# Performance work log

Measured on AMD Instinct MI355X. Metric: run time of the kernel, lower is better.

Reference implementation:

```python
import jax, jax.numpy as jnp
import numpy as np

INTRINSIC_DIM = 3  # all linear dims, no periodic dims
EPS = 1e-10


def _cdist(a, b):
    # Euclidean distance via the expanded form; clamp for numerical safety.
    sq = (jnp.sum(a * a, axis=1)[:, None]
          + jnp.sum(b * b, axis=1)[None, :]
          - 2.0 * (a @ b.T))
    return jnp.sqrt(jnp.maximum(sq, 0.0))


def _thin_plate_kernel(r, dim):
    r_safe = jnp.maximum(r, EPS)
    if dim == 2:
        k = r_safe ** 2 * jnp.log(r_safe)
    else:
        k = r_safe ** (dim - 2) * jnp.log(r_safe)
    return jnp.where(r < EPS, jnp.zeros_like(k), k)


def setup_inputs() -> dict:
    key = jax.random.key(0)
    k1, k2, k3, k4 = jax.random.split(key, 4)
    batch, n, d, amb = 16384, 4096, INTRINSIC_DIM, 3
    m = 1 + d  # constant + one linear term per (non-periodic) dim
    u = jax.random.uniform(k1, (batch, d), dtype=jnp.float32)
    control_points = jax.random.uniform(k2, (n, d), dtype=jnp.float32)
    rbf_weights = jax.random.normal(k3, (n, amb), dtype=jnp.float32)
    poly_coeffs = jax.random.normal(k4, (m, amb), dtype=jnp.float32)
    return {"u": u, "control_points": control_points,
            "rbf_weights": rbf_weights, "poly_coeffs": poly_coeffs}


def reference(u, control_points, rbf_weights, poly_coeffs):
    # K_query: (batch, n) TPS kernel on pairwise Euclidean distances
    dists = _cdist(u, control_points)
    K_query = _thin_plate_kernel(dists, dim=INTRINSIC_DIM)
    # Polynomial matrix: [1, x] over all linear dims -> (batch, 1 + d)
    P_query = jnp.concatenate([jnp.ones((u.shape[0], 1), dtype=u.dtype), u], axis=1)
    return K_query @ rbf_weights + P_query @ poly_coeffs
```

## Files before the change

### kernel.cpp

```cpp
#include <hip/hip_runtime.h>


#define BLK 256
#define NS 4
#define QPT 2
#define QPB 128
#define JCHUNK 256
#define JW (JCHUNK / NS)

__global__ __launch_bounds__(BLK, 8) void tps_kernel(
    const float* __restrict__ u,
    const float* __restrict__ cp,
    const float* __restrict__ w,
    const float* __restrict__ poly,
    float* __restrict__ out,
    int batch, int n)
{
    __shared__ float4 s_a[JCHUNK];
    __shared__ float4 s_b[JCHUNK];
    __shared__ float  s_red[NS][QPB * 3];

    const float C = 0.34657359027997264f;

    const int tid = threadIdx.x;
    const int j0 = blockIdx.y * JCHUNK;

    {
        const int g = j0 + tid;
        const float cx = cp[g * 3 + 0], cy = cp[g * 3 + 1], cz = cp[g * 3 + 2];
        s_a[tid] = make_float4(-2.f * cx, -2.f * cy, -2.f * cz,
                               fmaf(cx, cx, fmaf(cy, cy, cz * cz)));
        s_b[tid] = make_float4(C * w[g * 3 + 0], C * w[g * 3 + 1],
                               C * w[g * 3 + 2], 0.f);
    }
    __syncthreads();

    const int lane = tid & 63;
    const int wv   = tid >> 6;

    float ux[QPT], uy[QPT], uz[QPT], usq[QPT];
    float ax[QPT], ay[QPT], az[QPT];
#pragma unroll
    for (int k = 0; k < QPT; ++k) {
        const int q = blockIdx.x * QPB + k * 64 + lane;
        ux[k] = u[q * 3 + 0];
        uy[k] = u[q * 3 + 1];
        uz[k] = u[q * 3 + 2];
        usq[k] = fmaf(ux[k], ux[k], fmaf(uy[k], uy[k], uz[k] * uz[k]));
        ax[k] = ay[k] = az[k] = 0.f;
    }

    if (blockIdx.y == 0 && wv == 0) {
#pragma unroll
        for (int k = 0; k < QPT; ++k) {
            ax[k] = poly[0] + ux[k] * poly[3] + uy[k] * poly[6] + uz[k] * poly[9];
            ay[k] = poly[1] + ux[k] * poly[4] + uy[k] * poly[7] + uz[k] * poly[10];
            az[k] = poly[2] + ux[k] * poly[5] + uy[k] * poly[8] + uz[k] * poly[11];
        }
    }

    const int jlo = wv * JW;
#pragma unroll 4
    for (int j = jlo; j < jlo + JW; ++j) {
        const float4 A = s_a[j];
        const float4 B = s_b[j];
#pragma unroll
        for (int k = 0; k < QPT; ++k) {
            float r2 = fmaf(A.x, ux[k],
                       fmaf(A.y, uy[k],
                       fmaf(A.z, uz[k], A.w + usq[k])));
            r2 = fmaxf(r2, 1e-30f);
            const float kk = __builtin_amdgcn_sqrtf(r2) *
                             __builtin_amdgcn_logf(r2);
            ax[k] = fmaf(kk, B.x, ax[k]);
            ay[k] = fmaf(kk, B.y, ay[k]);
            az[k] = fmaf(kk, B.z, az[k]);
        }
    }

#pragma unroll
    for (int k = 0; k < QPT; ++k) {
        const int base = (k * 64 + lane) * 3;
        s_red[wv][base + 0] = ax[k];
        s_red[wv][base + 1] = ay[k];
        s_red[wv][base + 2] = az[k];
    }
    __syncthreads();

    for (int v = tid; v < QPB * 3; v += BLK) {
        float s = s_red[0][v] + s_red[1][v] + s_red[2][v] + s_red[3][v];
        atomicAdd(&out[(size_t)blockIdx.x * (QPB * 3) + v], s);
    }
}

extern "C" void kernel_launch(void* const* d_in, const int* in_sizes, int n_in,
                              void* d_out, int out_size, void* d_ws, size_t ws_size,
                              hipStream_t stream) {
    const float* u    = (const float*)d_in[0];
    const float* cp   = (const float*)d_in[1];
    const float* w    = (const float*)d_in[2];
    const float* poly = (const float*)d_in[3];
    float* out = (float*)d_out;

    const int batch = in_sizes[0] / 3;
    const int n     = in_sizes[1] / 3;

    hipMemsetAsync(d_out, 0, (size_t)out_size * sizeof(float), stream);

    dim3 block(BLK);
    dim3 grid(batch / QPB, n / JCHUNK);
    tps_kernel<<<grid, block, 0, stream>>>(u, cp, w, poly, out, batch, n);
}
```

Measured before the change: 80.32 us.

## Precompute packed control-point table and stream it via scalar loads

Adds a small pre-pass kernel that packs the scaled control-point terms and weights into an 8-float-per-point table in workspace. The main kernel then reads that table through wave-uniform scalar loads (s_load_dwordx16) into SGPRs instead of staging through LDS with a block barrier. This removes the per-block shared-memory fill, the __syncthreads and the LDS reads from the inner loop. In exchange it adds an extra kernel launch, and each 4-point group waits on its scalar loads with s_waitcnt lgkmcnt(0) and no prefetching, which can stall the wave.

Result: slower. 83.35 us (+3.8%).

```diff
diff --git a/kernel.cpp b/kernel.cpp
--- a/kernel.cpp
+++ b/kernel.cpp
@@ -8,35 +8,37 @@
 #define JCHUNK 256
 #define JW (JCHUNK / NS)
 
+typedef __attribute__((ext_vector_type(16))) int v16i;
+
+__global__ void pack_kernel(const float* __restrict__ cp,
+                            const float* __restrict__ w,
+                            float* __restrict__ pack, int n) {
+    const int j = blockIdx.x * blockDim.x + threadIdx.x;
+    if (j >= n) return;
+    const float C = 0.34657359027997264f;
+    const float cx = cp[j * 3 + 0], cy = cp[j * 3 + 1], cz = cp[j * 3 + 2];
+    pack[j * 8 + 0] = -2.f * cx;
+    pack[j * 8 + 1] = -2.f * cy;
+    pack[j * 8 + 2] = -2.f * cz;
+    pack[j * 8 + 3] = fmaf(cx, cx, fmaf(cy, cy, cz * cz));
+    pack[j * 8 + 4] = C * w[j * 3 + 0];
+    pack[j * 8 + 5] = C * w[j * 3 + 1];
+    pack[j * 8 + 6] = C * w[j * 3 + 2];
+    pack[j * 8 + 7] = 0.f;
+}
+
 __global__ __launch_bounds__(BLK, 8) void tps_kernel(
     const float* __restrict__ u,
-    const float* __restrict__ cp,
-    const float* __restrict__ w,
+    const float* __restrict__ pack,
     const float* __restrict__ poly,
     float* __restrict__ out,
     int batch, int n)
 {
-    __shared__ float4 s_a[JCHUNK];
-    __shared__ float4 s_b[JCHUNK];
-    __shared__ float  s_red[NS][QPB * 3];
+    __shared__ float s_red[NS][QPB * 3];
 
-    const float C = 0.34657359027997264f;
-
-    const int tid = threadIdx.x;
-    const int j0 = blockIdx.y * JCHUNK;
-
-    {
-        const int g = j0 + tid;
-        const float cx = cp[g * 3 + 0], cy = cp[g * 3 + 1], cz = cp[g * 3 + 2];
-        s_a[tid] = make_float4(-2.f * cx, -2.f * cy, -2.f * cz,
-                               fmaf(cx, cx, fmaf(cy, cy, cz * cz)));
-        s_b[tid] = make_float4(C * w[g * 3 + 0], C * w[g * 3 + 1],
-                               C * w[g * 3 + 2], 0.f);
-    }
-    __syncthreads();
-
+    const int tid  = threadIdx.x;
     const int lane = tid & 63;
-    const int wv   = tid >> 6;
+    const int wv   = __builtin_amdgcn_readfirstlane(tid >> 6);
 
     float ux[QPT], uy[QPT], uz[QPT], usq[QPT];
     float ax[QPT], ay[QPT], az[QPT];
@@ -59,22 +61,40 @@
         }
     }
 
-    const int jlo = wv * JW;
-#pragma unroll 4
-    for (int j = jlo; j < jlo + JW; ++j) {
-        const float4 A = s_a[j];
-        const float4 B = s_b[j];
+    const int jlo = blockIdx.y * JCHUNK + wv * JW;
+    const float* pj = pack + (size_t)jlo * 8;
+
+    for (int jj = 0; jj < JW; jj += 4) {
+        v16i d0, d1;
+        asm volatile("s_load_dwordx16 %0, %2, 0x0\n\t"
+                     "s_load_dwordx16 %1, %2, 0x40\n\t"
+                     "s_waitcnt lgkmcnt(0)"
+                     : "=s"(d0), "=s"(d1)
+                     : "s"(pj + (size_t)jj * 8)
+                     : "memory");
 #pragma unroll
-        for (int k = 0; k < QPT; ++k) {
-            float r2 = fmaf(A.x, ux[k],
-                       fmaf(A.y, uy[k],
-                       fmaf(A.z, uz[k], A.w + usq[k])));
-            r2 = fmaxf(r2, 1e-30f);
-            const float kk = __builtin_amdgcn_sqrtf(r2) *
-                             __builtin_amdgcn_logf(r2);
-            ax[k] = fmaf(kk, B.x, ax[k]);
-            ay[k] = fmaf(kk, B.y, ay[k]);
-            az[k] = fmaf(kk, B.z, az[k]);
+        for (int r = 0; r < 4; ++r) {
+            const v16i& d = (r < 2) ? d0 : d1;
+            const int o = (r & 1) * 8;
+            const float m2x = __int_as_float(d[o + 0]);
+            const float m2y = __int_as_float(d[o + 1]);
+            const float m2z = __int_as_float(d[o + 2]);
+            const float c2  = __int_as_float(d[o + 3]);
+            const float wx  = __int_as_float(d[o + 4]);
+            const float wy  = __int_as_float(d[o + 5]);
+            const float wz  = __int_as_float(d[o + 6]);
+#pragma unroll
+            for (int k = 0; k < QPT; ++k) {
+                float r2 = fmaf(m2x, ux[k],
+                           fmaf(m2y, uy[k],
+                           fmaf(m2z, uz[k], c2 + usq[k])));
+                r2 = fmaxf(r2, 1e-30f);
+                const float kk = __builtin_amdgcn_sqrtf(r2) *
+                                 __builtin_amdgcn_logf(r2);
+                ax[k] = fmaf(kk, wx, ax[k]);
+                ay[k] = fmaf(kk, wy, ay[k]);
+                az[k] = fmaf(kk, wz, az[k]);
+            }
         }
     }
 
@@ -100,14 +120,17 @@
     const float* cp   = (const float*)d_in[1];
     const float* w    = (const float*)d_in[2];
     const float* poly = (const float*)d_in[3];
-    float* out = (float*)d_out;
+    float* out  = (float*)d_out;
+    float* pack = (float*)d_ws;
 
     const int batch = in_sizes[0] / 3;
     const int n     = in_sizes[1] / 3;
+
+    pack_kernel<<<(n + 255) / 256, 256, 0, stream>>>(cp, w, pack, n);
 
     hipMemsetAsync(d_out, 0, (size_t)out_size * sizeof(float), stream);
 
     dim3 block(BLK);
     dim3 grid(batch / QPB, n / JCHUNK);
-    tps_kernel<<<grid, block, 0, stream>>>(u, cp, w, poly, out, batch, n);
+    tps_kernel<<<grid, block, 0, stream>>>(u, pack, poly, out, batch, n);
 }
```
